# Kernel optimization log

Hardware: AMD Instinct MI355X
Metric: run time of the kernel (lower is better)

Reference implementation:

```python
import jax
import jax.numpy as jnp
from jax import lax
import numpy as np


def design_butter_hp_sos(order: int, cutoff: float, fs: float) -> np.ndarray:
    """Pure-numpy replica of scipy.signal.butter(order, cutoff, 'hp', fs=fs, output='sos')."""
    Wn = cutoff / (fs / 2.0)          # normalized to Nyquist
    fs_b = 2.0                        # scipy's internal sampling rate convention
    warped = 2.0 * fs_b * np.tan(np.pi * Wn / fs_b)  # prewarped analog cutoff
    # Analog Butterworth lowpass prototype poles (buttap)
    m = np.arange(-order + 1, order, 2)
    p_lp = -np.exp(1j * np.pi * m / (2 * order))
    k = np.real(np.prod(-p_lp))       # == 1 for Butterworth
    # lp2hp: zeros at s=0, poles -> warped / p
    p_hp = warped / p_lp
    z_hp = np.zeros(order, dtype=complex)
    # bilinear transform (fs2 = 2 * fs_b)
    fs2 = 2.0 * fs_b
    p_z = (fs2 + p_hp) / (fs2 - p_hp)
    k_z = k * np.real(np.prod(fs2 - z_hp) / np.prod(fs2 - p_hp))
    # pair conjugate poles into biquads; scipy puts poles nearest unit circle LAST
    pos = p_z[np.imag(p_z) > 0]
    pos = pos[np.argsort(np.abs(pos))]
    n_sec = order // 2
    sos = np.zeros((n_sec, 6))
    for i, p in enumerate(pos):
        b = np.array([1.0, -2.0, 1.0])  # two zeros at z = 1 (DC block)
        if i == 0:
            b = b * k_z                 # overall gain lives in the first section
        sos[i, :3] = b
        sos[i, 3:] = np.array([1.0, -2.0 * p.real, np.abs(p) ** 2])
    return sos.astype(np.float32)


def setup_inputs() -> dict:
    key = jax.random.key(0)
    audio = jax.random.normal(key, (64, 480000), dtype=jnp.float32)  # [batch, samples]
    sos = jnp.asarray(design_butter_hp_sos(4, 80.0, 16000.0))        # [2, 6]
    return {"audio": audio, "sos": sos}


def _sosfilt(sos, x):
    """Cascade biquad IIR (direct form II transposed), zero initial state.
    x: [B, T], sos: [n_sections, 6]. Batch is vectorized inside the scan carry."""
    B = x.shape[0]

    def one_section(x, coefs):
        b0, b1, b2, _, a1, a2 = coefs

        def step(state, xn):
            s0, s1 = state                 # each [B]
            y = b0 * xn + s0
            s0_new = b1 * xn - a1 * y + s1
            s1_new = b2 * xn - a2 * y
            return (s0_new, s1_new), y

        init = (jnp.zeros(B, x.dtype), jnp.zeros(B, x.dtype))
        _, y = lax.scan(step, init, x.T)   # scan over time, [T, B]
        return y.T

    for i in range(sos.shape[0]):          # small static loop over 2 sections
        x = one_section(x, sos[i])
    return x


def reference(audio, sos):
    squeeze = audio.ndim == 1
    x = audio[None, :] if squeeze else audio
    y = _sosfilt(sos, x)
    return y[0] if squeeze else y
```

## Files before the change

kernel.cpp:

```cpp
#include <hip/hip_runtime.h>


#define SEG   32
#define F4S   (SEG / 4)
#define NT    32
#define SEGS  256
#define EMITS (SEGS - NT)

typedef float f32x4 __attribute__((ext_vector_type(4)));

struct Coefs { float b00,b01,b02,a01,a02,b10,b11,b12,a11,a12; };

__device__ __forceinline__ void step(const Coefs& c, float xn,
    float& s10, float& s11, float& s20, float& s21, float& yout) {
  float y1 = fmaf(c.b00, xn, s10);
  s10 = fmaf(-c.a01, y1, fmaf(c.b01, xn, s11));
  s11 = fmaf(-c.a02, y1, c.b02 * xn);
  float y2 = fmaf(c.b10, y1, s20);
  s20 = fmaf(-c.a11, y2, fmaf(c.b11, y1, s21));
  s21 = fmaf(-c.a12, y2, c.b12 * y1);
  yout = y2;
}

__device__ __forceinline__ Coefs load_coefs(const float* __restrict__ sos) {
  Coefs c;
  c.b00=sos[0]; c.b01=sos[1]; c.b02=sos[2]; c.a01=sos[4];  c.a02=sos[5];
  c.b10=sos[6]; c.b11=sos[7]; c.b12=sos[8]; c.a11=sos[10]; c.a12=sos[11];
  return c;
}

__global__ void iir_setup(const float* __restrict__ sos, float* __restrict__ ws) {
  if (blockIdx.x != 0 || threadIdx.x != 0) return;
  Coefs c = load_coefs(sos);
  float P[16];
  {
    float A[16];
    for (int col = 0; col < 4; ++col) {
      float a0 = (col == 0), a1 = (col == 1), a2 = (col == 2), a3 = (col == 3), dd;
      step(c, 0.f, a0, a1, a2, a3, dd);
      A[0*4+col] = a0; A[1*4+col] = a1; A[2*4+col] = a2; A[3*4+col] = a3;
    }
    for (int i = 0; i < 16; ++i) P[i] = A[i];
    for (int it = 0; it < 5; ++it) {
      float Q[16];
      for (int r = 0; r < 4; ++r)
        for (int cc = 0; cc < 4; ++cc) {
          float acc = 0.f;
          for (int kk = 0; kk < 4; ++kk) acc = fmaf(P[r*4+kk], P[kk*4+cc], acc);
          Q[r*4+cc] = acc;
        }
      for (int i = 0; i < 16; ++i) P[i] = Q[i];
    }
  }
  for (int l = 0; l < 5; ++l) {
    for (int i = 0; i < 16; ++i) ws[l*16 + i] = P[i];
    float Q[16];
    for (int r = 0; r < 4; ++r)
      for (int cc = 0; cc < 4; ++cc) {
        float acc = 0.f;
        for (int kk = 0; kk < 4; ++kk) acc = fmaf(P[r*4+kk], P[kk*4+cc], acc);
        Q[r*4+cc] = acc;
      }
    for (int i = 0; i < 16; ++i) P[i] = Q[i];
  }
}

__global__ __launch_bounds__(256, 4) void iir_fused(
    const float* __restrict__ x, const float* __restrict__ sos,
    const float* __restrict__ ws, float* __restrict__ out,
    int T, int nchunks, int bpr) {
  __shared__ f32x4 stg[SEGS * F4S];
  __shared__ f32x4 va[SEGS];
  __shared__ f32x4 vb[SEGS];

  int row = blockIdx.x / bpr;
  int blk = blockIdx.x - row * bpr;
  int k = threadIdx.x;
  int sbase = blk * EMITS - NT;
  int myseg = sbase + k;
  int perm = k & 7;
  Coefs c = load_coefs(sos);

  const f32x4* xr4 = reinterpret_cast<const f32x4*>(x) + (size_t)row * (T >> 2);
  f32x4*       yr4 = reinterpret_cast<f32x4*>(out)     + (size_t)row * (T >> 2);
  const f32x4 z4 = {0.f, 0.f, 0.f, 0.f};

  f32x4 t0,t1,t2,t3,t4,t5,t6,t7;
#define PREF(IT, TR) { int f_ = k + IT*256; int s_ = f_>>3; int gs_ = sbase + s_; \
    TR = (gs_ >= 0 && gs_ < nchunks) ? xr4[(size_t)gs_ * F4S + (f_&7)] : z4; }
#define WST(IT, TR) { int f_ = k + IT*256; int s_ = f_>>3, j_ = f_&7; \
    stg[s_*F4S + (j_^(s_&7))] = TR; }
  PREF(0,t0) PREF(1,t1) PREF(2,t2) PREF(3,t3)
  PREF(4,t4) PREF(5,t5) PREF(6,t6) PREF(7,t7)
  WST(0,t0) WST(1,t1) WST(2,t2) WST(3,t3)
  WST(4,t4) WST(5,t5) WST(6,t6) WST(7,t7)
  __syncthreads();

  {
    float s10 = 0.f, s11 = 0.f, s20 = 0.f, s21 = 0.f, d_;
#pragma unroll
    for (int j = 0; j < F4S; ++j) {
      f32x4 v = stg[k * F4S + (j ^ perm)];
      step(c, v[0], s10, s11, s20, s21, d_);
      step(c, v[1], s10, s11, s20, s21, d_);
      step(c, v[2], s10, s11, s20, s21, d_);
      step(c, v[3], s10, s11, s20, s21, d_);
    }
    f32x4 uu; uu[0] = s10; uu[1] = s11; uu[2] = s20; uu[3] = s21;
    va[k] = uu;
  }
  __syncthreads();

  {
    f32x4 vprev = (k >= 1) ? va[k - 1] : z4;
    __syncthreads();
    va[k] = vprev;
  }
  __syncthreads();

  {
    f32x4* src = va;
    f32x4* dst = vb;
#pragma unroll
    for (int l = 0; l < 5; ++l) {
      float p0  = ws[l*16+0],  p1  = ws[l*16+1],  p2  = ws[l*16+2],  p3  = ws[l*16+3];
      float p4  = ws[l*16+4],  p5  = ws[l*16+5],  p6  = ws[l*16+6],  p7  = ws[l*16+7];
      float p8  = ws[l*16+8],  p9  = ws[l*16+9],  p10 = ws[l*16+10], p11 = ws[l*16+11];
      float p12 = ws[l*16+12], p13 = ws[l*16+13], p14 = ws[l*16+14], p15 = ws[l*16+15];
      f32x4 mine = src[k];
      int off = 1 << l;
      f32x4 r = mine;
      if (k >= off) {
        f32x4 w = src[k - off];
        r[0] = mine[0] + fmaf(p0,  w[0], fmaf(p1,  w[1], fmaf(p2,  w[2], p3  * w[3])));
        r[1] = mine[1] + fmaf(p4,  w[0], fmaf(p5,  w[1], fmaf(p6,  w[2], p7  * w[3])));
        r[2] = mine[2] + fmaf(p8,  w[0], fmaf(p9,  w[1], fmaf(p10, w[2], p11 * w[3])));
        r[3] = mine[3] + fmaf(p12, w[0], fmaf(p13, w[1], fmaf(p14, w[2], p15 * w[3])));
      }
      dst[k] = r;
      __syncthreads();
      f32x4* tmp = src; src = dst; dst = tmp;
    }
    va[k] = src[k];
  }
  __syncthreads();

  bool emits = (k >= NT) && (myseg < nchunks);
  if (emits) {
    f32x4 s = va[k];
    float s10 = s[0], s11 = s[1], s20 = s[2], s21 = s[3];
#pragma unroll
    for (int j = 0; j < F4S; ++j) {
      f32x4 v = stg[k * F4S + (j ^ perm)];
      f32x4 yv; float yo;
      step(c, v[0], s10, s11, s20, s21, yo); yv[0] = yo;
      step(c, v[1], s10, s11, s20, s21, yo); yv[1] = yo;
      step(c, v[2], s10, s11, s20, s21, yo); yv[2] = yo;
      step(c, v[3], s10, s11, s20, s21, yo); yv[3] = yo;
      stg[k * F4S + (j ^ perm)] = yv;
    }
  }
  __syncthreads();

  int eseg0 = blk * EMITS;
  int nemit = nchunks - eseg0; if (nemit > EMITS) nemit = EMITS;
  if (nemit > 0) {
    int F = nemit * F4S;
    f32x4* dst = yr4 + (size_t)eseg0 * F4S;
    for (int f = k; f < F; f += 256) {
      int s = f >> 3, j = f & 7;
      int ls = s + NT;
      dst[f] = stg[ls * F4S + (j ^ (ls & 7))];
    }
  }
}

#define FB_C 256
#define FB_W 1024
__global__ __launch_bounds__(256) void sosfilt2_chunked(
    const float* __restrict__ x, const float* __restrict__ sos,
    float* __restrict__ out, int B, int T, int nchunks) {
  int tid = blockIdx.x * 256 + threadIdx.x;
  if (tid >= B * nchunks) return;
  int row = tid / nchunks;
  int chunk = tid - row * nchunks;
  Coefs c = load_coefs(sos);
  const float* xr = x + (size_t)row * T;
  float*       yr = out + (size_t)row * T;
  int c0   = chunk * FB_C;
  int cend = min(c0 + FB_C, T);
  int warm = min(FB_W, c0);
  int t    = c0 - warm;
  float s10 = 0.f, s11 = 0.f, s20 = 0.f, s21 = 0.f;
  float dump;
  for (; t < c0; t += 4) {
    f32x4 xvv = *reinterpret_cast<const f32x4*>(xr + t);
#pragma unroll
    for (int j = 0; j < 4; ++j) step(c, xvv[j], s10, s11, s20, s21, dump);
  }
  int tv_end = c0 + ((cend - c0) & ~3);
  for (; t < tv_end; t += 4) {
    f32x4 xvv = *reinterpret_cast<const f32x4*>(xr + t);
    f32x4 yv;
#pragma unroll
    for (int j = 0; j < 4; ++j) {
      float yo;
      step(c, xvv[j], s10, s11, s20, s21, yo);
      yv[j] = yo;
    }
    *reinterpret_cast<f32x4*>(yr + t) = yv;
  }
  for (; t < cend; ++t) { float yv; step(c, xr[t], s10, s11, s20, s21, yv); yr[t] = yv; }
}

extern "C" void kernel_launch(void* const* d_in, const int* in_sizes, int n_in,
                              void* d_out, int out_size, void* d_ws, size_t ws_size,
                              hipStream_t stream) {
  const float* x   = (const float*)d_in[0];
  const float* sos = (const float*)d_in[1];
  float*       out = (float*)d_out;

  int total = in_sizes[0];
  int T = 480000;
  if (total % T != 0) T = total;
  int B = total / T;

  if (T % SEG == 0 && ws_size >= 80 * sizeof(float)) {
    float* ws = (float*)d_ws;
    int nchunks = T / SEG;
    int bpr = (nchunks + EMITS - 1) / EMITS;
    iir_setup<<<1, 64, 0, stream>>>(sos, ws);
    iir_fused<<<B * bpr, 256, 0, stream>>>(x, sos, ws, out, T, nchunks, bpr);
  } else {
    int nc = (T + FB_C - 1) / FB_C;
    int grid = (B * nc + 255) / 256;
    sosfilt2_chunked<<<grid, 256, 0, stream>>>(x, sos, out, B, T, nc);
  }
}
```

Before: 52.17 us.

## Halve segment length, widen warmup, add scan level and drop shift pass

```diff
diff --git a/kernel.cpp b/kernel.cpp
--- a/kernel.cpp
+++ b/kernel.cpp
@@ -1,11 +1,12 @@
 #include <hip/hip_runtime.h>
 
 
-#define SEG   32
+#define SEG   16
 #define F4S   (SEG / 4)
-#define NT    32
+#define NT    64
 #define SEGS  256
 #define EMITS (SEGS - NT)
+#define NLVL  6
 
 typedef float f32x4 __attribute__((ext_vector_type(4)));
 
@@ -41,7 +42,7 @@
       A[0*4+col] = a0; A[1*4+col] = a1; A[2*4+col] = a2; A[3*4+col] = a3;
     }
     for (int i = 0; i < 16; ++i) P[i] = A[i];
-    for (int it = 0; it < 5; ++it) {
+    for (int it = 0; it < 4; ++it) {
       float Q[16];
       for (int r = 0; r < 4; ++r)
         for (int cc = 0; cc < 4; ++cc) {
@@ -52,7 +53,7 @@
       for (int i = 0; i < 16; ++i) P[i] = Q[i];
     }
   }
-  for (int l = 0; l < 5; ++l) {
+  for (int l = 0; l < NLVL; ++l) {
     for (int i = 0; i < 16; ++i) ws[l*16 + i] = P[i];
     float Q[16];
     for (int r = 0; r < 4; ++r)
@@ -65,7 +66,9 @@
   }
 }
 
-__global__ __launch_bounds__(256, 4) void iir_fused(
+#define SLOT(S, J) (((J) + ((S) >> 1)) & 3)
+
+__global__ __launch_bounds__(256, 6) void iir_fused(
     const float* __restrict__ x, const float* __restrict__ sos,
     const float* __restrict__ ws, float* __restrict__ out,
     int T, int nchunks, int bpr) {
@@ -78,43 +81,34 @@
   int k = threadIdx.x;
   int sbase = blk * EMITS - NT;
   int myseg = sbase + k;
-  int perm = k & 7;
   Coefs c = load_coefs(sos);
 
   const f32x4* xr4 = reinterpret_cast<const f32x4*>(x) + (size_t)row * (T >> 2);
   f32x4*       yr4 = reinterpret_cast<f32x4*>(out)     + (size_t)row * (T >> 2);
   const f32x4 z4 = {0.f, 0.f, 0.f, 0.f};
 
-  f32x4 t0,t1,t2,t3,t4,t5,t6,t7;
-#define PREF(IT, TR) { int f_ = k + IT*256; int s_ = f_>>3; int gs_ = sbase + s_; \
-    TR = (gs_ >= 0 && gs_ < nchunks) ? xr4[(size_t)gs_ * F4S + (f_&7)] : z4; }
-#define WST(IT, TR) { int f_ = k + IT*256; int s_ = f_>>3, j_ = f_&7; \
-    stg[s_*F4S + (j_^(s_&7))] = TR; }
+  f32x4 t0, t1, t2, t3;
+#define PREF(IT, TR) { int f_ = k + IT*256; int s_ = f_>>2; int gs_ = sbase + s_; \
+    TR = (gs_ >= 0 && gs_ < nchunks) ? xr4[(size_t)gs_ * F4S + (f_&3)] : z4; }
+#define WST(IT, TR) { int f_ = k + IT*256; int s_ = f_>>2, j_ = f_&3; \
+    stg[s_*F4S + SLOT(s_, j_)] = TR; }
   PREF(0,t0) PREF(1,t1) PREF(2,t2) PREF(3,t3)
-  PREF(4,t4) PREF(5,t5) PREF(6,t6) PREF(7,t7)
   WST(0,t0) WST(1,t1) WST(2,t2) WST(3,t3)
-  WST(4,t4) WST(5,t5) WST(6,t6) WST(7,t7)
   __syncthreads();
 
+  f32x4 mine;
   {
     float s10 = 0.f, s11 = 0.f, s20 = 0.f, s21 = 0.f, d_;
 #pragma unroll
     for (int j = 0; j < F4S; ++j) {
-      f32x4 v = stg[k * F4S + (j ^ perm)];
+      f32x4 v = stg[k * F4S + SLOT(k, j)];
       step(c, v[0], s10, s11, s20, s21, d_);
       step(c, v[1], s10, s11, s20, s21, d_);
       step(c, v[2], s10, s11, s20, s21, d_);
       step(c, v[3], s10, s11, s20, s21, d_);
     }
-    f32x4 uu; uu[0] = s10; uu[1] = s11; uu[2] = s20; uu[3] = s21;
-    va[k] = uu;
-  }
-  __syncthreads();
-
-  {
-    f32x4 vprev = (k >= 1) ? va[k - 1] : z4;
-    __syncthreads();
-    va[k] = vprev;
+    mine[0] = s10; mine[1] = s11; mine[2] = s20; mine[3] = s21;
+    va[k] = mine;
   }
   __syncthreads();
 
@@ -122,42 +116,35 @@
     f32x4* src = va;
     f32x4* dst = vb;
 #pragma unroll
-    for (int l = 0; l < 5; ++l) {
-      float p0  = ws[l*16+0],  p1  = ws[l*16+1],  p2  = ws[l*16+2],  p3  = ws[l*16+3];
-      float p4  = ws[l*16+4],  p5  = ws[l*16+5],  p6  = ws[l*16+6],  p7  = ws[l*16+7];
-      float p8  = ws[l*16+8],  p9  = ws[l*16+9],  p10 = ws[l*16+10], p11 = ws[l*16+11];
-      float p12 = ws[l*16+12], p13 = ws[l*16+13], p14 = ws[l*16+14], p15 = ws[l*16+15];
-      f32x4 mine = src[k];
+    for (int l = 0; l < NLVL; ++l) {
       int off = 1 << l;
-      f32x4 r = mine;
       if (k >= off) {
+        const float* pw = ws + l * 16;
         f32x4 w = src[k - off];
-        r[0] = mine[0] + fmaf(p0,  w[0], fmaf(p1,  w[1], fmaf(p2,  w[2], p3  * w[3])));
-        r[1] = mine[1] + fmaf(p4,  w[0], fmaf(p5,  w[1], fmaf(p6,  w[2], p7  * w[3])));
-        r[2] = mine[2] + fmaf(p8,  w[0], fmaf(p9,  w[1], fmaf(p10, w[2], p11 * w[3])));
-        r[3] = mine[3] + fmaf(p12, w[0], fmaf(p13, w[1], fmaf(p14, w[2], p15 * w[3])));
+        mine[0] += fmaf(pw[0],  w[0], fmaf(pw[1],  w[1], fmaf(pw[2],  w[2], pw[3]  * w[3])));
+        mine[1] += fmaf(pw[4],  w[0], fmaf(pw[5],  w[1], fmaf(pw[6],  w[2], pw[7]  * w[3])));
+        mine[2] += fmaf(pw[8],  w[0], fmaf(pw[9],  w[1], fmaf(pw[10], w[2], pw[11] * w[3])));
+        mine[3] += fmaf(pw[12], w[0], fmaf(pw[13], w[1], fmaf(pw[14], w[2], pw[15] * w[3])));
       }
-      dst[k] = r;
+      dst[k] = mine;
       __syncthreads();
       f32x4* tmp = src; src = dst; dst = tmp;
     }
-    va[k] = src[k];
-  }
-  __syncthreads();
+  }
 
   bool emits = (k >= NT) && (myseg < nchunks);
   if (emits) {
-    f32x4 s = va[k];
-    float s10 = s[0], s11 = s[1], s20 = s[2], s21 = s[3];
+    f32x4 sv = va[k - 1];
+    float s10 = sv[0], s11 = sv[1], s20 = sv[2], s21 = sv[3];
 #pragma unroll
     for (int j = 0; j < F4S; ++j) {
-      f32x4 v = stg[k * F4S + (j ^ perm)];
+      f32x4 v = stg[k * F4S + SLOT(k, j)];
       f32x4 yv; float yo;
       step(c, v[0], s10, s11, s20, s21, yo); yv[0] = yo;
       step(c, v[1], s10, s11, s20, s21, yo); yv[1] = yo;
       step(c, v[2], s10, s11, s20, s21, yo); yv[2] = yo;
       step(c, v[3], s10, s11, s20, s21, yo); yv[3] = yo;
-      stg[k * F4S + (j ^ perm)] = yv;
+      stg[k * F4S + SLOT(k, j)] = yv;
     }
   }
   __syncthreads();
@@ -168,9 +155,9 @@
     int F = nemit * F4S;
     f32x4* dst = yr4 + (size_t)eseg0 * F4S;
     for (int f = k; f < F; f += 256) {
-      int s = f >> 3, j = f & 7;
+      int s = f >> 2, j = f & 3;
       int ls = s + NT;
-      dst[f] = stg[ls * F4S + (j ^ (ls & 7))];
+      dst[f] = stg[ls * F4S + SLOT(ls, j)];
     }
   }
 }
@@ -225,7 +212,7 @@
   if (total % T != 0) T = total;
   int B = total / T;
 
-  if (T % SEG == 0 && ws_size >= 80 * sizeof(float)) {
+  if (T % SEG == 0 && ws_size >= (size_t)(NLVL * 16) * sizeof(float)) {
     float* ws = (float*)d_ws;
     int nchunks = T / SEG;
     int bpr = (nchunks + EMITS - 1) / EMITS;
```

Measured after the change: 53.80 us. 3.1% more time.

## Replace shared-memory Hillis-Steele state scan with wavefront shuffle scan

Applied to the files above, without the earlier changes.

```diff
diff --git a/kernel.cpp b/kernel.cpp
--- a/kernel.cpp
+++ b/kernel.cpp
@@ -2,10 +2,11 @@
 
 
 #define SEG   32
-#define F4S   (SEG / 4)
+#define F4S   8
 #define NT    32
 #define SEGS  256
 #define EMITS (SEGS - NT)
+#define NWAVE 4
 
 typedef float f32x4 __attribute__((ext_vector_type(4)));
 
@@ -27,6 +28,15 @@
   c.b00=sos[0]; c.b01=sos[1]; c.b02=sos[2]; c.a01=sos[4];  c.a02=sos[5];
   c.b10=sos[6]; c.b11=sos[7]; c.b12=sos[8]; c.a11=sos[10]; c.a12=sos[11];
   return c;
+}
+
+__device__ __forceinline__ f32x4 matvec(const float* __restrict__ m, f32x4 v) {
+  f32x4 r;
+  r[0] = fmaf(m[0],  v[0], fmaf(m[1],  v[1], fmaf(m[2],  v[2], m[3]  * v[3])));
+  r[1] = fmaf(m[4],  v[0], fmaf(m[5],  v[1], fmaf(m[6],  v[2], m[7]  * v[3])));
+  r[2] = fmaf(m[8],  v[0], fmaf(m[9],  v[1], fmaf(m[10], v[2], m[11] * v[3])));
+  r[3] = fmaf(m[12], v[0], fmaf(m[13], v[1], fmaf(m[14], v[2], m[15] * v[3])));
+  return r;
 }
 
 __global__ void iir_setup(const float* __restrict__ sos, float* __restrict__ ws) {
@@ -52,7 +62,7 @@
       for (int i = 0; i < 16; ++i) P[i] = Q[i];
     }
   }
-  for (int l = 0; l < 5; ++l) {
+  for (int l = 0; l < 7; ++l) {
     for (int i = 0; i < 16; ++i) ws[l*16 + i] = P[i];
     float Q[16];
     for (int r = 0; r < 4; ++r)
@@ -70,12 +80,12 @@
     const float* __restrict__ ws, float* __restrict__ out,
     int T, int nchunks, int bpr) {
   __shared__ f32x4 stg[SEGS * F4S];
-  __shared__ f32x4 va[SEGS];
-  __shared__ f32x4 vb[SEGS];
+  __shared__ f32x4 wtot[NWAVE];
 
   int row = blockIdx.x / bpr;
   int blk = blockIdx.x - row * bpr;
   int k = threadIdx.x;
+  int lane = k & 63, wid = k >> 6;
   int sbase = blk * EMITS - NT;
   int myseg = sbase + k;
   int perm = k & 7;
@@ -96,6 +106,7 @@
   WST(4,t4) WST(5,t5) WST(6,t6) WST(7,t7)
   __syncthreads();
 
+  f32x4 u;
   {
     float s10 = 0.f, s11 = 0.f, s20 = 0.f, s21 = 0.f, d_;
 #pragma unroll
@@ -106,49 +117,67 @@
       step(c, v[2], s10, s11, s20, s21, d_);
       step(c, v[3], s10, s11, s20, s21, d_);
     }
-    f32x4 uu; uu[0] = s10; uu[1] = s11; uu[2] = s20; uu[3] = s21;
-    va[k] = uu;
-  }
+    u[0] = s10; u[1] = s11; u[2] = s20; u[3] = s21;
+  }
+
+  f32x4 I = u;
+#pragma unroll
+  for (int l = 0; l < 6; ++l) {
+    int off = 1 << l;
+    f32x4 w;
+    w[0] = __shfl_up(I[0], off, 64);
+    w[1] = __shfl_up(I[1], off, 64);
+    w[2] = __shfl_up(I[2], off, 64);
+    w[3] = __shfl_up(I[3], off, 64);
+    if (lane >= off) {
+      f32x4 pv = matvec(ws + l * 16, w);
+      I[0] += pv[0]; I[1] += pv[1]; I[2] += pv[2]; I[3] += pv[3];
+    }
+  }
+  if (lane == 63) wtot[wid] = I;
   __syncthreads();
 
-  {
-    f32x4 vprev = (k >= 1) ? va[k - 1] : z4;
-    __syncthreads();
-    va[k] = vprev;
-  }
-  __syncthreads();
-
-  {
-    f32x4* src = va;
-    f32x4* dst = vb;
-#pragma unroll
-    for (int l = 0; l < 5; ++l) {
-      float p0  = ws[l*16+0],  p1  = ws[l*16+1],  p2  = ws[l*16+2],  p3  = ws[l*16+3];
-      float p4  = ws[l*16+4],  p5  = ws[l*16+5],  p6  = ws[l*16+6],  p7  = ws[l*16+7];
-      float p8  = ws[l*16+8],  p9  = ws[l*16+9],  p10 = ws[l*16+10], p11 = ws[l*16+11];
-      float p12 = ws[l*16+12], p13 = ws[l*16+13], p14 = ws[l*16+14], p15 = ws[l*16+15];
-      f32x4 mine = src[k];
-      int off = 1 << l;
-      f32x4 r = mine;
-      if (k >= off) {
-        f32x4 w = src[k - off];
-        r[0] = mine[0] + fmaf(p0,  w[0], fmaf(p1,  w[1], fmaf(p2,  w[2], p3  * w[3])));
-        r[1] = mine[1] + fmaf(p4,  w[0], fmaf(p5,  w[1], fmaf(p6,  w[2], p7  * w[3])));
-        r[2] = mine[2] + fmaf(p8,  w[0], fmaf(p9,  w[1], fmaf(p10, w[2], p11 * w[3])));
-        r[3] = mine[3] + fmaf(p12, w[0], fmaf(p13, w[1], fmaf(p14, w[2], p15 * w[3])));
+  f32x4 carry = z4;
+  if (wid > 0) {
+    carry = wtot[0];
+    const float* p64 = ws + 6 * 16;
+#pragma unroll
+    for (int p = 1; p < NWAVE - 1; ++p)
+      if (p <= wid - 1) {
+        f32x4 pc = matvec(p64, carry);
+        carry[0] = wtot[p][0] + pc[0]; carry[1] = wtot[p][1] + pc[1];
+        carry[2] = wtot[p][2] + pc[2]; carry[3] = wtot[p][3] + pc[3];
       }
-      dst[k] = r;
-      __syncthreads();
-      f32x4* tmp = src; src = dst; dst = tmp;
-    }
-    va[k] = src[k];
-  }
-  __syncthreads();
+  }
+
+  if (lane == 0) {
+    f32x4 pc = matvec(ws, carry);
+    u[0] += pc[0]; u[1] += pc[1]; u[2] += pc[2]; u[3] += pc[3];
+  }
+  I = u;
+#pragma unroll
+  for (int l = 0; l < 6; ++l) {
+    int off = 1 << l;
+    f32x4 w;
+    w[0] = __shfl_up(I[0], off, 64);
+    w[1] = __shfl_up(I[1], off, 64);
+    w[2] = __shfl_up(I[2], off, 64);
+    w[3] = __shfl_up(I[3], off, 64);
+    if (lane >= off) {
+      f32x4 pv = matvec(ws + l * 16, w);
+      I[0] += pv[0]; I[1] += pv[1]; I[2] += pv[2]; I[3] += pv[3];
+    }
+  }
+  f32x4 S;
+  S[0] = __shfl_up(I[0], 1, 64);
+  S[1] = __shfl_up(I[1], 1, 64);
+  S[2] = __shfl_up(I[2], 1, 64);
+  S[3] = __shfl_up(I[3], 1, 64);
+  if (lane == 0) S = carry;
 
   bool emits = (k >= NT) && (myseg < nchunks);
   if (emits) {
-    f32x4 s = va[k];
-    float s10 = s[0], s11 = s[1], s20 = s[2], s21 = s[3];
+    float s10 = S[0], s11 = S[1], s20 = S[2], s21 = S[3];
 #pragma unroll
     for (int j = 0; j < F4S; ++j) {
       f32x4 v = stg[k * F4S + (j ^ perm)];
@@ -225,7 +254,7 @@
   if (total % T != 0) T = total;
   int B = total / T;
 
-  if (T % SEG == 0 && ws_size >= 80 * sizeof(float)) {
+  if (T % SEG == 0 && ws_size >= 112 * sizeof(float)) {
     float* ws = (float*)d_ws;
     int nchunks = T / SEG;
     int bpr = (nchunks + EMITS - 1) / EMITS;
```

Result: slower. 54.54 us (+4.6%).
